# Kernel tuning notes

Hardware: AMD Instinct MI355X
Metric: run time of the kernel (lower is better)

The kernel has to match this reference:

```python
import jax, jax.numpy as jnp
import numpy as np

N = 10000
E = 160000
D = 512
EDGE_DIM = 128
L = 3
LN_EPS = 1e-5


def setup_inputs() -> dict:
    key = jax.random.key(0)
    ks = jax.random.split(key, 16)
    s = 0.02
    return {
        "x": jax.random.normal(ks[0], (N, D), dtype=jnp.float32),
        "edge_index": jax.random.randint(ks[1], (2, E), 0, N, dtype=jnp.int64),
        "edge_attr": jax.random.normal(ks[2], (E, EDGE_DIM), dtype=jnp.float32),
        # per-layer GINEConv edge projection Linear(edge_dim -> d_in); here d_in == D for all layers
        "We": jax.random.normal(ks[3], (L, EDGE_DIM, D), dtype=jnp.float32) * s,
        "be": jnp.zeros((L, D), dtype=jnp.float32),
        "eps": jnp.zeros((L,), dtype=jnp.float32),  # train_eps=True, init 0
        # per-layer MLP: Linear(D->D), ReLU, Linear(D->D)
        "W1": jax.random.normal(ks[4], (L, D, D), dtype=jnp.float32) * s,
        "b1": jnp.zeros((L, D), dtype=jnp.float32),
        "W2": jax.random.normal(ks[5], (L, D, D), dtype=jnp.float32) * s,
        "b2": jnp.zeros((L, D), dtype=jnp.float32),
        # per-layer LayerNorm
        "gamma": jnp.ones((L, D), dtype=jnp.float32),
        "beta": jnp.zeros((L, D), dtype=jnp.float32),
        # final Linear(D->D)
        "Wf": jax.random.normal(ks[6], (D, D), dtype=jnp.float32) * s,
        "bf": jnp.zeros((D,), dtype=jnp.float32),
    }


def reference(x, edge_index, edge_attr, We, be, eps, W1, b1, W2, b2, gamma, beta, Wf, bf):
    src = edge_index[0]  # x_j (source)
    dst = edge_index[1]  # aggregation target i
    n = x.shape[0]
    h = x
    for l in range(L):
        # GINEConv message: relu(x_j + lin(edge_attr)), scatter-add at dst
        e = jax.nn.relu(h[src] + edge_attr @ We[l] + be[l])  # [E, D]
        agg = jax.ops.segment_sum(e, dst, num_segments=n)     # [N, D]
        g = (1.0 + eps[l]) * h + agg
        # 2-layer MLP
        g = jax.nn.relu(g @ W1[l] + b1[l]) @ W2[l] + b2[l]
        # ReLU then LayerNorm (dropout p=0)
        g = jax.nn.relu(g)
        mu = jnp.mean(g, axis=-1, keepdims=True)
        var = jnp.mean(jnp.square(g - mu), axis=-1, keepdims=True)
        h = (g - mu) * jax.lax.rsqrt(var + LN_EPS) * gamma[l] + beta[l]
    return h @ Wf + bf
```

## Files before the change

kernel.cpp:

```cpp
#include <hip/hip_runtime.h>

#define NN 10000
#define EE 160000
#define DD 512
#define EDIM 128
#define LLAYERS 3
#define LN_EPS 1e-5f

typedef __attribute__((ext_vector_type(8))) short bf16x8;
typedef __attribute__((ext_vector_type(4))) float f32x4;
typedef __attribute__((ext_vector_type(4))) unsigned int u32x4;

__device__ __forceinline__ unsigned short f2b(float f) {
    union { float f; unsigned u; } v; v.f = f;
    unsigned r = (v.u + 0x7fffu + ((v.u >> 16) & 1u)) >> 16;
    return (unsigned short)r;
}
__device__ __forceinline__ float b2f(unsigned short s) {
    union { unsigned u; float f; } v; v.u = ((unsigned)s) << 16;
    return v.f;
}
__device__ __forceinline__ unsigned short f2h(float f) {
    _Float16 h = (_Float16)f;
    unsigned short u; __builtin_memcpy(&u, &h, 2);
    return u;
}
__device__ __forceinline__ float h2f(unsigned short u) {
    _Float16 h; __builtin_memcpy(&h, &u, 2);
    return (float)h;
}

__global__ __launch_bounds__(256) void hist_kernel(
    const int* __restrict__ dstv, int* __restrict__ deg)
{
    int e = blockIdx.x * 256 + threadIdx.x;
    if (e < EE) atomicAdd(&deg[dstv[e]], 1);
}

__global__ __launch_bounds__(256) void scan_kernel(
    const int* __restrict__ deg, int* __restrict__ base, int* __restrict__ cursor)
{
    __shared__ int sums[256];
    const int t = threadIdx.x;
    const int CH = 40;
    int lo = t * CH;
    int hi = lo + CH; if (hi > NN) hi = NN;
    int s = 0;
    for (int i = lo; i < hi; i++) s += deg[i];
    sums[t] = s;
    __syncthreads();
    for (int off = 1; off < 256; off <<= 1) {
        int v = (t >= off) ? sums[t - off] : 0;
        __syncthreads();
        sums[t] += v;
        __syncthreads();
    }
    int run = (t == 0) ? 0 : sums[t - 1];
    for (int i = lo; i < hi; i++) {
        base[i] = run; cursor[i] = run;
        run += deg[i];
    }
}

__global__ __launch_bounds__(256) void scatter_kernel(
    const int* __restrict__ srcv, const int* __restrict__ dstv,
    int* __restrict__ cursor,
    int* __restrict__ ssrc, int* __restrict__ sdst, int* __restrict__ perm)
{
    int e = blockIdx.x * 256 + threadIdx.x;
    if (e < EE) {
        int d = dstv[e];
        int pos = atomicAdd(&cursor[d], 1);
        ssrc[pos] = srcv[e];
        sdst[pos] = d;
        perm[pos] = e;
    }
}

__global__ __launch_bounds__(256) void transpose_bf16_kernel(
    const float* __restrict__ src, unsigned short* __restrict__ dst, int K, int N)
{
    __shared__ float t[32][33];
    const int x = threadIdx.x & 31;
    const int y = threadIdx.x >> 5;
    const int bn = blockIdx.x * 32;
    const int bk = blockIdx.y * 32;
    #pragma unroll
    for (int j = 0; j < 32; j += 8)
        t[y + j][x] = src[(size_t)(bk + y + j) * N + bn + x];
    __syncthreads();
    #pragma unroll
    for (int j = 0; j < 32; j += 8)
        dst[(size_t)(bn + y + j) * K + bk + x] = f2b(t[x][y + j]);
}

__global__ __launch_bounds__(256) void cvt_bf16_kernel(
    const float* __restrict__ src, unsigned short* __restrict__ dst)
{
    int i = blockIdx.x * 256 + threadIdx.x;
    float4 v = ((const float4*)src)[i];
    uint2 o;
    o.x = (unsigned)f2b(v.x) | ((unsigned)f2b(v.y) << 16);
    o.y = (unsigned)f2b(v.z) | ((unsigned)f2b(v.w) << 16);
    ((uint2*)dst)[i] = o;
}

__global__ __launch_bounds__(256) void gather_cvt_kernel(
    const float* __restrict__ ea, const int* __restrict__ perm,
    unsigned short* __restrict__ out, int elo)
{
    int i = blockIdx.x * 256 + threadIdx.x;
    int r = i >> 5, c4 = (i & 31) * 4;
    const float* p = ea + (size_t)perm[elo + r] * EDIM + c4;
    float4 v = *(const float4*)p;
    uint2 o;
    o.x = (unsigned)f2b(v.x) | ((unsigned)f2b(v.y) << 16);
    o.y = (unsigned)f2b(v.z) | ((unsigned)f2b(v.w) << 16);
    *(uint2*)&out[(size_t)r * EDIM + c4] = o;
}

#define MEP 136

__global__ __launch_bounds__(256) void msg_gemm(
    const unsigned short* __restrict__ Abf,
    const unsigned short* __restrict__ WeT,
    const float* __restrict__ be,
    unsigned short* __restrict__ msg)
{
    __shared__ unsigned short sA[128 * MEP];

    const int tid  = threadIdx.x;
    const int c0   = blockIdx.x * 128;
    const int e0   = blockIdx.y * 128;
    const int w    = tid >> 6;
    const int lane = tid & 63;
    const int quad = lane >> 4;
    const int l16  = lane & 15;
    const int mh   = (w & 1) * 64;
    const int nsl  = (w >> 1) * 64;

    for (int i = tid; i < 128 * 16; i += 256) {
        int r = i >> 4, seg = i & 15;
        *(u32x4*)&sA[r * MEP + seg * 8] =
            *(const u32x4*)&Abf[(size_t)(e0 + r) * EDIM + seg * 8];
    }
    __syncthreads();

    f32x4 acc[4][4];
    #pragma unroll
    for (int mr = 0; mr < 4; mr++)
        #pragma unroll
        for (int nb = 0; nb < 4; nb++)
            acc[mr][nb] = (f32x4){0.f, 0.f, 0.f, 0.f};

    #pragma unroll
    for (int ks = 0; ks < 4; ks++) {
        const int ko = ks * 32 + quad * 8;
        bf16x8 a[4];
        #pragma unroll
        for (int mr = 0; mr < 4; mr++)
            a[mr] = *(const bf16x8*)&sA[(mh + mr * 16 + l16) * MEP + ko];
        bf16x8 b[4];
        #pragma unroll
        for (int nb = 0; nb < 4; nb++)
            b[nb] = *(const bf16x8*)&WeT[(size_t)(c0 + nsl + nb * 16 + l16) * EDIM + ko];
        #pragma unroll
        for (int mr = 0; mr < 4; mr++)
            #pragma unroll
            for (int nb = 0; nb < 4; nb++)
                acc[mr][nb] = __builtin_amdgcn_mfma_f32_16x16x32_bf16(a[mr], b[nb], acc[mr][nb], 0, 0, 0);
    }

    __syncthreads();
    #pragma unroll
    for (int mr = 0; mr < 4; mr++) {
        const int lr = mh + mr * 16 + quad * 4;
        #pragma unroll
        for (int nb = 0; nb < 4; nb++) {
            const int lc = nsl + nb * 16 + l16;
            const float bv = be[c0 + lc];
            const f32x4 v = acc[mr][nb];
            #pragma unroll
            for (int reg = 0; reg < 4; reg++)
                sA[(lr + reg) * MEP + lc] = f2h(v[reg] + bv);
        }
    }
    __syncthreads();
    for (int i = tid; i < 128 * 16; i += 256) {
        int r = i >> 4, seg = i & 15;
        *(u32x4*)&msg[(size_t)(e0 + r) * DD + c0 + seg * 8] =
            *(const u32x4*)&sA[r * MEP + seg * 8];
    }
}

__global__ __launch_bounds__(256) void agg_kernel(
    const unsigned short* __restrict__ h_bf,
    const unsigned short* __restrict__ msg,
    const int* __restrict__ ssrc,
    const int* __restrict__ basep,
    const int* __restrict__ degp,
    const float* __restrict__ epsp,
    float* __restrict__ aggp,
    unsigned short* __restrict__ aprime,
    int elo, int ehi, int first, int last)
{
    const int d  = blockIdx.x;
    const int b0 = basep[d];
    const int b1 = b0 + degp[d];
    int lo = b0 > elo ? b0 : elo;
    int hi = b1 < ehi ? b1 : ehi;
    if (!first && !last && lo >= hi) return;

    const int t  = threadIdx.x;
    const int c2 = t * 2;

    float a0 = 0.f, a1 = 0.f;
    if (!first) {
        float2 pv = *(const float2*)&aggp[(size_t)d * DD + c2];
        a0 = pv.x; a1 = pv.y;
    }
    int p = lo;
    for (; p + 4 <= hi; p += 4) {
        const int s0 = ssrc[p],     s1 = ssrc[p + 1];
        const int s2 = ssrc[p + 2], s3 = ssrc[p + 3];
        unsigned m0v = *(const unsigned*)&msg[(size_t)(p     - elo) * DD + c2];
        unsigned m1v = *(const unsigned*)&msg[(size_t)(p + 1 - elo) * DD + c2];
        unsigned m2v = *(const unsigned*)&msg[(size_t)(p + 2 - elo) * DD + c2];
        unsigned m3v = *(const unsigned*)&msg[(size_t)(p + 3 - elo) * DD + c2];
        unsigned h0v = *(const unsigned*)&h_bf[(size_t)s0 * DD + c2];
        unsigned h1v = *(const unsigned*)&h_bf[(size_t)s1 * DD + c2];
        unsigned h2v = *(const unsigned*)&h_bf[(size_t)s2 * DD + c2];
        unsigned h3v = *(const unsigned*)&h_bf[(size_t)s3 * DD + c2];
        a0 += fmaxf(h2f((unsigned short)(m0v & 0xffffu)) + b2f((unsigned short)(h0v & 0xffffu)), 0.f);
        a1 += fmaxf(h2f((unsigned short)(m0v >> 16))     + b2f((unsigned short)(h0v >> 16)),     0.f);
        a0 += fmaxf(h2f((unsigned short)(m1v & 0xffffu)) + b2f((unsigned short)(h1v & 0xffffu)), 0.f);
        a1 += fmaxf(h2f((unsigned short)(m1v >> 16))     + b2f((unsigned short)(h1v >> 16)),     0.f);
        a0 += fmaxf(h2f((unsigned short)(m2v & 0xffffu)) + b2f((unsigned short)(h2v & 0xffffu)), 0.f);
        a1 += fmaxf(h2f((unsigned short)(m2v >> 16))     + b2f((unsigned short)(h2v >> 16)),     0.f);
        a0 += fmaxf(h2f((unsigned short)(m3v & 0xffffu)) + b2f((unsigned short)(h3v & 0xffffu)), 0.f);
        a1 += fmaxf(h2f((unsigned short)(m3v >> 16))     + b2f((unsigned short)(h3v >> 16)),     0.f);
    }
    for (; p < hi; p++) {
        const int s = ssrc[p];
        unsigned mv = *(const unsigned*)&msg[(size_t)(p - elo) * DD + c2];
        unsigned hv = *(const unsigned*)&h_bf[(size_t)s * DD + c2];
        a0 += fmaxf(h2f((unsigned short)(mv & 0xffffu)) + b2f((unsigned short)(hv & 0xffffu)), 0.f);
        a1 += fmaxf(h2f((unsigned short)(mv >> 16))     + b2f((unsigned short)(hv >> 16)),     0.f);
    }
    if (last) {
        const float es = 1.0f + epsp[0];
        unsigned hv = *(const unsigned*)&h_bf[(size_t)d * DD + c2];
        unsigned o = (unsigned)f2b(es * b2f((unsigned short)(hv & 0xffffu)) + a0)
                   | ((unsigned)f2b(es * b2f((unsigned short)(hv >> 16))    + a1) << 16);
        *(unsigned*)&aprime[(size_t)d * DD + c2] = o;
    } else {
        *(float2*)&aggp[(size_t)d * DD + c2] = make_float2(a0, a1);
    }
}

#define GP 136
template <bool RELU, bool F32OUT>
__global__ __launch_bounds__(256) void gemm64(
    const unsigned short* __restrict__ A,
    const unsigned short* __restrict__ WT,
    const float* __restrict__ bias,
    void* __restrict__ Cout, int M)
{
    __shared__ unsigned short sA[64 * GP];

    const int tid  = threadIdx.x;
    const int c0   = blockIdx.x * 64;
    const int m0   = blockIdx.y * 64;
    const int w    = tid >> 6;
    const int lane = tid & 63;
    const int quad = lane >> 4;
    const int l16  = lane & 15;
    const int mh   = (w & 1) * 32;
    const int nsl  = (w >> 1) * 32;

    f32x4 acc[2][2];
    #pragma unroll
    for (int mr = 0; mr < 2; mr++)
        #pragma unroll
        for (int nb = 0; nb < 2; nb++)
            acc[mr][nb] = (f32x4){0.f, 0.f, 0.f, 0.f};

    for (int kc = 0; kc < DD; kc += 128) {
        if (kc) __syncthreads();
        #pragma unroll
        for (int i = tid; i < 64 * 16; i += 256) {
            int r = i >> 4, seg = i & 15;
            int gm = m0 + r;
            u32x4 v = (u32x4){0u, 0u, 0u, 0u};
            if (gm < M)
                v = *(const u32x4*)&A[(size_t)gm * DD + kc + seg * 8];
            *(u32x4*)&sA[r * GP + seg * 8] = v;
        }
        __syncthreads();
        #pragma unroll
        for (int ks = 0; ks < 4; ks++) {
            const int ko = ks * 32 + quad * 8;
            bf16x8 a0 = *(const bf16x8*)&sA[(mh + l16) * GP + ko];
            bf16x8 a1 = *(const bf16x8*)&sA[(mh + 16 + l16) * GP + ko];
            bf16x8 b0 = *(const bf16x8*)&WT[(size_t)(c0 + nsl + l16) * DD + kc + ko];
            bf16x8 b1 = *(const bf16x8*)&WT[(size_t)(c0 + nsl + 16 + l16) * DD + kc + ko];
            acc[0][0] = __builtin_amdgcn_mfma_f32_16x16x32_bf16(a0, b0, acc[0][0], 0, 0, 0);
            acc[0][1] = __builtin_amdgcn_mfma_f32_16x16x32_bf16(a0, b1, acc[0][1], 0, 0, 0);
            acc[1][0] = __builtin_amdgcn_mfma_f32_16x16x32_bf16(a1, b0, acc[1][0], 0, 0, 0);
            acc[1][1] = __builtin_amdgcn_mfma_f32_16x16x32_bf16(a1, b1, acc[1][1], 0, 0, 0);
        }
    }

    #pragma unroll
    for (int mr = 0; mr < 2; mr++) {
        const int rb = m0 + mh + mr * 16 + quad * 4;
        #pragma unroll
        for (int nb = 0; nb < 2; nb++) {
            const int cc = c0 + nsl + nb * 16 + l16;
            const float bv = bias[cc];
            const f32x4 v = acc[mr][nb];
            #pragma unroll
            for (int reg = 0; reg < 4; reg++) {
                int gm = rb + reg;
                if (gm < M) {
                    float val = v[reg] + bv;
                    if (RELU) val = fmaxf(val, 0.f);
                    if (F32OUT) ((float*)Cout)[(size_t)gm * DD + cc] = val;
                    else ((unsigned short*)Cout)[(size_t)gm * DD + cc] = f2b(val);
                }
            }
        }
    }
}

__global__ __launch_bounds__(256) void relu_ln_kernel(
    const unsigned short* __restrict__ g2,
    const float* __restrict__ gamma,
    const float* __restrict__ beta,
    unsigned short* __restrict__ hout)
{
    __shared__ float ss[4], ssq[4];
    const int row = blockIdx.x;
    const int t   = threadIdx.x;
    const unsigned* gr = (const unsigned*)(g2 + (size_t)row * DD);

    unsigned gv = gr[t];
    float v0 = fmaxf(b2f((unsigned short)(gv & 0xffffu)), 0.f);
    float v1 = fmaxf(b2f((unsigned short)(gv >> 16)),     0.f);
    float s  = v0 + v1;
    float sq = v0 * v0 + v1 * v1;
    #pragma unroll
    for (int off = 32; off > 0; off >>= 1) {
        s  += __shfl_down(s, off);
        sq += __shfl_down(sq, off);
    }
    const int wave = t >> 6;
    const int lane = t & 63;
    if (lane == 0) { ss[wave] = s; ssq[wave] = sq; }
    __syncthreads();
    if (t == 0) {
        float S  = ss[0] + ss[1] + ss[2] + ss[3];
        float SQ = ssq[0] + ssq[1] + ssq[2] + ssq[3];
        float mu = S * (1.f / 512.f);
        float var = SQ * (1.f / 512.f) - mu * mu;
        ss[0]  = mu;
        ssq[0] = rsqrtf(var + LN_EPS);
    }
    __syncthreads();
    float mu = ss[0], rstd = ssq[0];
    unsigned o = (unsigned)f2b((v0 - mu) * rstd * gamma[2 * t] + beta[2 * t])
               | ((unsigned)f2b((v1 - mu) * rstd * gamma[2 * t + 1] + beta[2 * t + 1]) << 16);
    ((unsigned*)(hout + (size_t)row * DD))[t] = o;
}

extern "C" void kernel_launch(void* const* d_in, const int* in_sizes, int n_in,
                              void* d_out, int out_size, void* d_ws, size_t ws_size,
                              hipStream_t stream)
{
    (void)in_sizes; (void)n_in; (void)out_size;

    const float* x          = (const float*)d_in[0];
    const int*   edge_index = (const int*)d_in[1];
    const float* edge_attr  = (const float*)d_in[2];
    const float* We         = (const float*)d_in[3];
    const float* be         = (const float*)d_in[4];
    const float* eps        = (const float*)d_in[5];
    const float* W1         = (const float*)d_in[6];
    const float* b1         = (const float*)d_in[7];
    const float* W2         = (const float*)d_in[8];
    const float* b2         = (const float*)d_in[9];
    const float* gamma      = (const float*)d_in[10];
    const float* beta       = (const float*)d_in[11];
    const float* Wf         = (const float*)d_in[12];
    const float* bf         = (const float*)d_in[13];

    unsigned short* h_bf   = (unsigned short*)d_ws;
    unsigned short* aprime = h_bf + (size_t)NN * DD;
    unsigned short* t1     = aprime + (size_t)NN * DD;
    unsigned short* t2     = t1 + (size_t)NN * DD;
    unsigned short* WeT    = t2 + (size_t)NN * DD;
    unsigned short* W1T    = WeT + (size_t)LLAYERS * DD * EDIM;
    unsigned short* W2T    = W1T + (size_t)LLAYERS * DD * DD;
    unsigned short* WfT    = W2T + (size_t)LLAYERS * DD * DD;
    int* deg    = (int*)(WfT + (size_t)DD * DD);
    int* basep  = deg + NN;
    int* cursor = basep + NN;
    int* ssrc   = cursor + NN;
    int* sdst   = ssrc + EE;
    int* perm   = sdst + EE;
    float* aggp = (float*)(perm + EE);
    unsigned short* ea_hf = (unsigned short*)(aggp + (size_t)NN * DD);

    size_t used = (size_t)((unsigned char*)ea_hf - (unsigned char*)d_ws);
    size_t rem  = ws_size > used ? ws_size - used : 0;
    const size_t EA_FULL  = (size_t)EE * EDIM * 2;
    const size_t MSG_FULL = (size_t)EE * DD * 2;
    int ea_full; long long capE;
    if (rem >= EA_FULL + MSG_FULL) {
        ea_full = 1; capE = EE;
    } else if (rem >= EA_FULL + (size_t)32 * 1024 * 1024) {
        ea_full = 1;
        capE = (long long)((rem - EA_FULL) / ((size_t)DD * 2)) & ~127LL;
    } else {
        ea_full = 0;
        capE = (long long)(rem / ((size_t)(EDIM + DD) * 2)) & ~127LL;
        if (capE < 128) capE = 128;
    }
    if (capE > EE) capE = EE;
    unsigned short* msg = ea_hf + (ea_full ? (size_t)EE * EDIM : (size_t)capE * EDIM);

    const int* srcv = edge_index;
    const int* dstv = edge_index + EE;

    hipMemsetAsync(deg, 0, NN * sizeof(int), stream);
    hist_kernel<<<dim3((EE + 255) / 256), 256, 0, stream>>>(dstv, deg);
    scan_kernel<<<dim3(1), 256, 0, stream>>>(deg, basep, cursor);
    scatter_kernel<<<dim3((EE + 255) / 256), 256, 0, stream>>>(
        srcv, dstv, cursor, ssrc, sdst, perm);

    cvt_bf16_kernel<<<dim3(NN * DD / 4 / 256), 256, 0, stream>>>(x, h_bf);
    for (int l = 0; l < LLAYERS; l++) {
        transpose_bf16_kernel<<<dim3(DD / 32, EDIM / 32), 256, 0, stream>>>(
            We + (size_t)l * EDIM * DD, WeT + (size_t)l * DD * EDIM, EDIM, DD);
        transpose_bf16_kernel<<<dim3(DD / 32, DD / 32), 256, 0, stream>>>(
            W1 + (size_t)l * DD * DD, W1T + (size_t)l * DD * DD, DD, DD);
        transpose_bf16_kernel<<<dim3(DD / 32, DD / 32), 256, 0, stream>>>(
            W2 + (size_t)l * DD * DD, W2T + (size_t)l * DD * DD, DD, DD);
    }
    transpose_bf16_kernel<<<dim3(DD / 32, DD / 32), 256, 0, stream>>>(Wf, WfT, DD, DD);

    if (ea_full)
        gather_cvt_kernel<<<dim3(EE / 8), 256, 0, stream>>>(edge_attr, perm, ea_hf, 0);

    dim3 ggrid64(DD / 64, (NN + 63) / 64);

    const int nch = (int)((EE + capE - 1) / capE);
    for (int l = 0; l < LLAYERS; l++) {
        for (int c = 0; c < nch; c++) {
            const int elo = (int)((long long)c * capE);
            const int cnt = (EE - elo < capE) ? (EE - elo) : (int)capE;
            if (!ea_full)
                gather_cvt_kernel<<<dim3(cnt / 8), 256, 0, stream>>>(edge_attr, perm, ea_hf, elo);
            const unsigned short* Ab = ea_full ? ea_hf + (size_t)elo * EDIM : ea_hf;
            msg_gemm<<<dim3(4, cnt / 128), 256, 0, stream>>>(
                Ab, WeT + (size_t)l * DD * EDIM, be + (size_t)l * DD, msg);
            agg_kernel<<<dim3(NN), 256, 0, stream>>>(
                h_bf, msg, ssrc, basep, deg, eps + l, aggp, aprime,
                elo, elo + cnt, c == 0 ? 1 : 0, c == nch - 1 ? 1 : 0);
        }
        gemm64<true, false><<<ggrid64, 256, 0, stream>>>(
            aprime, W1T + (size_t)l * DD * DD, b1 + (size_t)l * DD, t1, NN);
        gemm64<false, false><<<ggrid64, 256, 0, stream>>>(
            t1, W2T + (size_t)l * DD * DD, b2 + (size_t)l * DD, t2, NN);
        relu_ln_kernel<<<dim3(NN), 256, 0, stream>>>(
            t2, gamma + (size_t)l * DD, beta + (size_t)l * DD, h_bf);
    }
    gemm64<false, true><<<ggrid64, 256, 0, stream>>>(h_bf, WfT, bf, d_out, NN);
}
```

Measured before the change: 859.3 us.

## Stage weight tiles in LDS with 64x128 GEMM tiles and cap edge chunk size

The dense GEMM now uses a 64x128 output tile per block and stages the transposed weight tile in shared memory, instead of having every wave read B fragments straight from global memory. The grid is reordered so M varies fastest, and each wave computes a 32x64 sub-tile. The aim is better reuse of the weights and fewer global loads, at the cost of more LDS per block and possibly lower occupancy. Separately, the edge chunk size is capped at 32768, which forces several msg_gemm/agg passes per layer and is probably meant to keep the message buffer resident in cache.

```diff
diff --git a/kernel.cpp b/kernel.cpp
--- a/kernel.cpp
+++ b/kernel.cpp
@@ -258,75 +258,83 @@
     }
 }
 
-#define GP 136
-template <bool RELU, bool F32OUT>
-__global__ __launch_bounds__(256) void gemm64(
+#define GPITCH 136
+template <bool RELU, bool OUTBF>
+__global__ __launch_bounds__(256) void mfma_gemm(
     const unsigned short* __restrict__ A,
     const unsigned short* __restrict__ WT,
     const float* __restrict__ bias,
     void* __restrict__ Cout, int M)
 {
-    __shared__ unsigned short sA[64 * GP];
+    __shared__ unsigned short sA[64 * GPITCH];
+    __shared__ unsigned short sB[128 * GPITCH];
 
     const int tid  = threadIdx.x;
-    const int c0   = blockIdx.x * 64;
-    const int m0   = blockIdx.y * 64;
+    const int m0   = blockIdx.x * 64;
+    const int c0   = blockIdx.y * 128;
     const int w    = tid >> 6;
     const int lane = tid & 63;
     const int quad = lane >> 4;
     const int l16  = lane & 15;
     const int mh   = (w & 1) * 32;
-    const int nsl  = (w >> 1) * 32;
-
-    f32x4 acc[2][2];
+    const int nsl  = (w >> 1) * 64;
+
+    f32x4 acc[2][4];
     #pragma unroll
     for (int mr = 0; mr < 2; mr++)
         #pragma unroll
-        for (int nb = 0; nb < 2; nb++)
+        for (int nb = 0; nb < 4; nb++)
             acc[mr][nb] = (f32x4){0.f, 0.f, 0.f, 0.f};
 
     for (int kc = 0; kc < DD; kc += 128) {
-        if (kc) __syncthreads();
-        #pragma unroll
+        __syncthreads();
         for (int i = tid; i < 64 * 16; i += 256) {
             int r = i >> 4, seg = i & 15;
             int gm = m0 + r;
             u32x4 v = (u32x4){0u, 0u, 0u, 0u};
             if (gm < M)
                 v = *(const u32x4*)&A[(size_t)gm * DD + kc + seg * 8];
-            *(u32x4*)&sA[r * GP + seg * 8] = v;
+            *(u32x4*)&sA[r * GPITCH + seg * 8] = v;
+        }
+        for (int i = tid; i < 128 * 16; i += 256) {
+            int r = i >> 4, seg = i & 15;
+            *(u32x4*)&sB[r * GPITCH + seg * 8] =
+                *(const u32x4*)&WT[(size_t)(c0 + r) * DD + kc + seg * 8];
         }
         __syncthreads();
         #pragma unroll
         for (int ks = 0; ks < 4; ks++) {
             const int ko = ks * 32 + quad * 8;
-            bf16x8 a0 = *(const bf16x8*)&sA[(mh + l16) * GP + ko];
-            bf16x8 a1 = *(const bf16x8*)&sA[(mh + 16 + l16) * GP + ko];
-            bf16x8 b0 = *(const bf16x8*)&WT[(size_t)(c0 + nsl + l16) * DD + kc + ko];
-            bf16x8 b1 = *(const bf16x8*)&WT[(size_t)(c0 + nsl + 16 + l16) * DD + kc + ko];
-            acc[0][0] = __builtin_amdgcn_mfma_f32_16x16x32_bf16(a0, b0, acc[0][0], 0, 0, 0);
-            acc[0][1] = __builtin_amdgcn_mfma_f32_16x16x32_bf16(a0, b1, acc[0][1], 0, 0, 0);
-            acc[1][0] = __builtin_amdgcn_mfma_f32_16x16x32_bf16(a1, b0, acc[1][0], 0, 0, 0);
-            acc[1][1] = __builtin_amdgcn_mfma_f32_16x16x32_bf16(a1, b1, acc[1][1], 0, 0, 0);
+            bf16x8 a0 = *(const bf16x8*)&sA[(mh + l16) * GPITCH + ko];
+            bf16x8 a1 = *(const bf16x8*)&sA[(mh + 16 + l16) * GPITCH + ko];
+            bf16x8 b[4];
+            #pragma unroll
+            for (int nb = 0; nb < 4; nb++)
+                b[nb] = *(const bf16x8*)&sB[(nsl + nb * 16 + l16) * GPITCH + ko];
+            #pragma unroll
+            for (int nb = 0; nb < 4; nb++) {
+                acc[0][nb] = __builtin_amdgcn_mfma_f32_16x16x32_bf16(a0, b[nb], acc[0][nb], 0, 0, 0);
+                acc[1][nb] = __builtin_amdgcn_mfma_f32_16x16x32_bf16(a1, b[nb], acc[1][nb], 0, 0, 0);
+            }
         }
     }
 
     #pragma unroll
     for (int mr = 0; mr < 2; mr++) {
-        const int rb = m0 + mh + mr * 16 + quad * 4;
-        #pragma unroll
-        for (int nb = 0; nb < 2; nb++) {
-            const int cc = c0 + nsl + nb * 16 + l16;
-            const float bv = bias[cc];
+        const int rbase = m0 + mh + mr * 16 + quad * 4;
+        #pragma unroll
+        for (int nb = 0; nb < 4; nb++) {
+            const int c = c0 + nsl + nb * 16 + l16;
+            const float bv = bias[c];
             const f32x4 v = acc[mr][nb];
             #pragma unroll
             for (int reg = 0; reg < 4; reg++) {
-                int gm = rb + reg;
+                int gm = rbase + reg;
                 if (gm < M) {
                     float val = v[reg] + bv;
                     if (RELU) val = fmaxf(val, 0.f);
-                    if (F32OUT) ((float*)Cout)[(size_t)gm * DD + cc] = val;
-                    else ((unsigned short*)Cout)[(size_t)gm * DD + cc] = f2b(val);
+                    if (OUTBF) ((unsigned short*)Cout)[(size_t)gm * DD + c] = f2b(val);
+                    else       ((float*)Cout)[(size_t)gm * DD + c] = val;
                 }
             }
         }
@@ -413,12 +421,9 @@
 
     size_t used = (size_t)((unsigned char*)ea_hf - (unsigned char*)d_ws);
     size_t rem  = ws_size > used ? ws_size - used : 0;
-    const size_t EA_FULL  = (size_t)EE * EDIM * 2;
-    const size_t MSG_FULL = (size_t)EE * DD * 2;
+    const size_t EA_FULL = (size_t)EE * EDIM * 2;
     int ea_full; long long capE;
-    if (rem >= EA_FULL + MSG_FULL) {
-        ea_full = 1; capE = EE;
-    } else if (rem >= EA_FULL + (size_t)32 * 1024 * 1024) {
+    if (rem >= EA_FULL + (size_t)32 * 1024 * 1024) {
         ea_full = 1;
         capE = (long long)((rem - EA_FULL) / ((size_t)DD * 2)) & ~127LL;
     } else {
@@ -426,6 +431,7 @@
         capE = (long long)(rem / ((size_t)(EDIM + DD) * 2)) & ~127LL;
         if (capE < 128) capE = 128;
     }
+    if (capE > 32768) capE = 32768;
     if (capE > EE) capE = EE;
     unsigned short* msg = ea_hf + (ea_full ? (size_t)EE * EDIM : (size_t)capE * EDIM);
 
@@ -452,7 +458,7 @@
     if (ea_full)
         gather_cvt_kernel<<<dim3(EE / 8), 256, 0, stream>>>(edge_attr, perm, ea_hf, 0);
 
-    dim3 ggrid64(DD / 64, (NN + 63) / 64);
+    dim3 ggrid((NN + 63) / 64, DD / 128);
 
     const int nch = (int)((EE + capE - 1) / capE);
     for (int l = 0; l < LLAYERS; l++) {
@@ -468,12 +474,12 @@
                 h_bf, msg, ssrc, basep, deg, eps + l, aggp, aprime,
                 elo, elo + cnt, c == 0 ? 1 : 0, c == nch - 1 ? 1 : 0);
         }
-        gemm64<true, false><<<ggrid64, 256, 0, stream>>>(
+        mfma_gemm<true, true><<<ggrid, 256, 0, stream>>>(
             aprime, W1T + (size_t)l * DD * DD, b1 + (size_t)l * DD, t1, NN);
-        gemm64<false, false><<<ggrid64, 256, 0, stream>>>(
+        mfma_gemm<false, true><<<ggrid, 256, 0, stream>>>(
             t1, W2T + (size_t)l * DD * DD, b2 + (size_t)l * DD, t2, NN);
         relu_ln_kernel<<<dim3(NN), 256, 0, stream>>>(
             t2, gamma + (size_t)l * DD, beta + (size_t)l * DD, h_bf);
     }
-    gemm64<false, true><<<ggrid64, 256, 0, stream>>>(h_bf, WfT, bf, d_out, NN);
-}
+    mfma_gemm<false, false><<<ggrid, 256, 0, stream>>>(h_bf, WfT, bf, d_out, NN);
+}
```

Measured after the change: 985.5 us. 14.7% more time.
